# Kernel optimization log

Hardware: AMD Instinct MI355X
Metric: run time of the kernel (lower is better)

Reference implementation:

```python
import jax, jax.numpy as jnp
import numpy as np


def _logcumsumexp(x, axis):
    return jax.lax.associative_scan(jnp.logaddexp, x, axis=axis)


def _log_g(x):
    # log of g(x) = where(x>=0, x+0.5, sigmoid(x))
    return jnp.where(x >= 0, jnp.log(jax.nn.relu(x) + 0.5), -jax.nn.softplus(-x))


def _min_gru(x, Wz, bz, Wh, bh):
    # x: [B, S, D_in] -> h: [B, S, H]; log-space Heinsen parallel scan over S
    k = x @ Wz + bz                      # gate pre-activation
    log_z = -jax.nn.softplus(-k)         # log(sigmoid(k))  = log z
    log_coeffs = -jax.nn.softplus(k)     # log(1 - sigmoid(k))
    log_tilde_h = _log_g(x @ Wh + bh)    # log candidate hidden
    a_star = jnp.cumsum(log_coeffs, axis=1)
    log_h = a_star + _logcumsumexp(log_z + log_tilde_h - a_star, axis=1)
    return jnp.exp(log_h)


def setup_inputs() -> dict:
    key = jax.random.key(0)
    ks = jax.random.split(key, 7)
    B, S, D, H = 4, 4096, 1024, 1024
    s_in = 1.0 / np.sqrt(D)
    s_cat = 1.0 / np.sqrt(2 * H)
    return {
        "x": jax.random.normal(ks[0], (B, S, D), jnp.float32),
        "Wz_f": jax.random.normal(ks[1], (D, H), jnp.float32) * s_in,
        "bz_f": jnp.zeros((H,), jnp.float32),
        "Wh_f": jax.random.normal(ks[2], (D, H), jnp.float32) * s_in,
        "bh_f": jnp.zeros((H,), jnp.float32),
        "Wz_b": jax.random.normal(ks[3], (D, H), jnp.float32) * s_in,
        "bz_b": jnp.zeros((H,), jnp.float32),
        "Wh_b": jax.random.normal(ks[4], (D, H), jnp.float32) * s_in,
        "bh_b": jnp.zeros((H,), jnp.float32),
        "W_out": jax.random.normal(ks[5], (2 * H, H), jnp.float32) * s_cat,
        "b_out": jnp.zeros((H,), jnp.float32),
    }


def reference(x, Wz_f, bz_f, Wh_f, bh_f, Wz_b, bz_b, Wh_b, bh_b, W_out, b_out):
    x_rev = jnp.flip(x, axis=1)
    out_fwd = _min_gru(x, Wz_f, bz_f, Wh_f, bh_f)        # [B, S, H]
    out_bwd = _min_gru(x_rev, Wz_b, bz_b, Wh_b, bh_b)    # [B, S, H] (not re-flipped, per source)
    concat = jnp.concatenate([out_fwd, out_bwd], axis=2)  # [B, S, 2H]
    return concat @ W_out + b_out                         # [B, S, H]
```

## Files before the change

### kernel.cpp

```cpp
#include <hip/hip_runtime.h>
#include <stdint.h>

typedef __attribute__((ext_vector_type(8))) short bf16x8;
typedef __attribute__((ext_vector_type(4))) float f32x4;
typedef __attribute__((ext_vector_type(4))) unsigned short u16x4;

#define SEQ 4096

__device__ __forceinline__ float bf2f(unsigned short u) {
  union { unsigned int i; float f; } v; v.i = ((unsigned int)u) << 16; return v.f;
}
__device__ __forceinline__ unsigned short f2bf(float f) {
  union { float f; unsigned int i; } v; v.f = f;
  unsigned int u = v.i;
  u = u + 0x7FFFu + ((u >> 16) & 1u);
  return (unsigned short)(u >> 16);
}
__device__ __forceinline__ float sigm(float x) { return 1.0f / (1.0f + __expf(-x)); }


__global__ void cvt_x_kernel(const float* __restrict__ in, unsigned short* __restrict__ out, int n8) {
  int i = blockIdx.x * blockDim.x + threadIdx.x;
  int stride = gridDim.x * blockDim.x;
  for (; i < n8; i += stride) {
    const float4* p = (const float4*)in + (size_t)i * 2;
    float4 a = p[0], b = p[1];
    union { unsigned short u[8]; uint4 v; } r;
    r.u[0] = f2bf(a.x); r.u[1] = f2bf(a.y); r.u[2] = f2bf(a.z); r.u[3] = f2bf(a.w);
    r.u[4] = f2bf(b.x); r.u[5] = f2bf(b.y); r.u[6] = f2bf(b.z); r.u[7] = f2bf(b.w);
    ((uint4*)out)[i] = r.v;
  }
}

__global__ void tconvb_kernel(const float* __restrict__ s0, const float* __restrict__ s1,
                              const float* __restrict__ s2, const float* __restrict__ s3,
                              const float* __restrict__ s4, unsigned short* __restrict__ WT4,
                              unsigned short* __restrict__ WTout) {
  __shared__ float t[32][33];
  int z = blockIdx.z;
  const float* src; unsigned short* dst; int K, k0;
  if (z < 4) {
    src = (z == 0) ? s0 : (z == 1) ? s1 : (z == 2) ? s2 : s3;
    dst = WT4 + (size_t)z * 1048576; K = 1024; k0 = blockIdx.y * 32;
  } else {
    src = s4; dst = WTout; K = 2048; k0 = blockIdx.y * 32 + (z - 4) * 1024;
  }
  int n0 = blockIdx.x * 32;
  int tx = threadIdx.x & 31, ty = threadIdx.x >> 5;
#pragma unroll
  for (int i = 0; i < 32; i += 8)
    t[ty + i][tx] = src[(size_t)(k0 + ty + i) * 1024 + n0 + tx];
  __syncthreads();
#pragma unroll
  for (int i = 0; i < 32; i += 8)
    dst[(size_t)(n0 + ty + i) * K + k0 + tx] = f2bf(t[tx][ty + i]);
}

__global__ void concat_bias_kernel(const float* b0, const float* b1, const float* b2,
                                   const float* b3, float* b4) {
  int i = blockIdx.x * 256 + threadIdx.x;
  const float* p = (i < 1024) ? b0 : (i < 2048) ? b1 : (i < 3072) ? b2 : b3;
  b4[i] = p[i & 1023];
}

template <int MODE>
__device__ __forceinline__ void store_frag(const f32x4& v, const float* bias, void* Cout,
                                           int col, int rb) {
  float bcol = bias[col];
  if (MODE == 0) {
    unsigned short* ACTp = (unsigned short*)Cout;
    bool isz = ((col >> 10) & 1) == 0;
#pragma unroll
    for (int r = 0; r < 4; ++r) {
      float x = v[r] + bcol;
      float res;
      if (isz) res = sigm(-x);
      else res = (x >= 0.f) ? (x + 0.5f) : sigm(x);
      ACTp[(size_t)(rb + r) * 4096 + col] = f2bf(res);
    }
  } else {
    float* Op = (float*)Cout;
#pragma unroll
    for (int r = 0; r < 4; ++r) Op[(size_t)(rb + r) * 1024 + col] = v[r] + bcol;
  }
}

#define DSR(D, A, OFFSTR) \
  asm volatile("ds_read_b128 %0, %1 offset:" OFFSTR : "=&v"(D) : "v"(A))

#define GLL(SRC, DIDX)                                                                  \
  __builtin_amdgcn_global_load_lds((const __attribute__((address_space(1))) void*)(SRC), \
                                   (__attribute__((address_space(3))) void*)&lds[DIDX], \
                                   16, 0, 0)

template <int MODE>
__global__ __launch_bounds__(512, 2) void gemm256_kernel(
    const unsigned short* __restrict__ A, const unsigned short* __restrict__ BT,
    const float* __restrict__ bias, void* __restrict__ Cout, int K, int NT) {
  __shared__ unsigned short lds[32768];

  const int tid = threadIdx.x;
  const int lane = tid & 63;
  const int wv = tid >> 6;
  const int wm = wv >> 2;
  const int wn = wv & 3;
  const int lo = lane & 15, hi = lane >> 4;

  const int nwg = gridDim.x;
  const int bid = blockIdx.x;
  const int cpx = nwg >> 3;
  const int sw = (bid & 7) * cpx + (bid >> 3);
  const int mt = sw / NT, nt = sw - mt * NT;
  const int m0 = mt << 8, n0 = nt << 8;

  const int srow = tid >> 2;
  const int skb = (((tid & 3) ^ ((tid >> 3) & 3)) << 4);
  const unsigned short* pA0 = A + (size_t)(m0 + srow) * K + (skb >> 1);
  const unsigned short* pA1 = pA0 + (size_t)128 * K;
  const unsigned short* pB0 = BT + (size_t)(n0 + srow) * K + (skb >> 1);
  const unsigned short* pB1 = pB0 + (size_t)128 * K;
  const int dstBase = wv << 9;

#define STAGE(KT, BUF)                                     \
  do {                                                     \
    const int ko_ = (KT) << 5;                             \
    GLL(pA0 + ko_, (BUF) * 8192 + dstBase);                \
    GLL(pA1 + ko_, (BUF) * 8192 + 4096 + dstBase);         \
    GLL(pB0 + ko_, 16384 + (BUF) * 8192 + dstBase);        \
    GLL(pB1 + ko_, 16384 + (BUF) * 8192 + 4096 + dstBase); \
  } while (0)

  f32x4 acc[8][4];
#pragma unroll
  for (int i = 0; i < 8; ++i)
#pragma unroll
    for (int j = 0; j < 4; ++j) acc[i][j] = (f32x4){0.f, 0.f, 0.f, 0.f};

  const int swz = ((lo >> 1) & 3) << 4;
  const int kof = ((hi << 4) ^ swz) >> 1;
  const unsigned ldsBase = (unsigned)(unsigned long long)&lds[0];
  const unsigned aByte = ldsBase + (unsigned)((((wm * 128 + lo) * 32) + kof) << 1);
  const unsigned bByte = ldsBase + 32768u + (unsigned)((((wn * 64 + lo) * 32) + kof) << 1);

  const int nT = K >> 5;
  STAGE(0, 0);
  for (int kt = 0; kt < nT; ++kt) {
    const int buf = kt & 1;
    if (kt + 1 < nT) {
      STAGE(kt + 1, buf ^ 1);
      asm volatile("s_waitcnt vmcnt(4)" ::: "memory");
    } else {
      asm volatile("s_waitcnt vmcnt(0)" ::: "memory");
    }
    __builtin_amdgcn_s_barrier();

    const unsigned aA = aByte + (unsigned)(buf << 14);
    const unsigned bA = bByte + (unsigned)(buf << 14);
    bf16x8 af0, af1, af2, af3, af4, af5, af6, af7, bf0, bf1, bf2, bf3;
    DSR(af0, aA, "0");    DSR(af1, aA, "1024");
    DSR(af2, aA, "2048"); DSR(af3, aA, "3072");
    DSR(af4, aA, "4096"); DSR(af5, aA, "5120");
    DSR(af6, aA, "6144"); DSR(af7, aA, "7168");
    DSR(bf0, bA, "0");    DSR(bf1, bA, "1024");
    DSR(bf2, bA, "2048"); DSR(bf3, bA, "3072");
    asm volatile("s_waitcnt lgkmcnt(0)" ::: "memory");
    __builtin_amdgcn_sched_barrier(0);
    __builtin_amdgcn_s_setprio(1);
#define MM(MI, NI) \
    acc[MI][NI] = __builtin_amdgcn_mfma_f32_16x16x32_bf16(af##MI, bf##NI, acc[MI][NI], 0, 0, 0)
    MM(0, 0); MM(0, 1); MM(0, 2); MM(0, 3);
    MM(1, 0); MM(1, 1); MM(1, 2); MM(1, 3);
    MM(2, 0); MM(2, 1); MM(2, 2); MM(2, 3);
    MM(3, 0); MM(3, 1); MM(3, 2); MM(3, 3);
    MM(4, 0); MM(4, 1); MM(4, 2); MM(4, 3);
    MM(5, 0); MM(5, 1); MM(5, 2); MM(5, 3);
    MM(6, 0); MM(6, 1); MM(6, 2); MM(6, 3);
    MM(7, 0); MM(7, 1); MM(7, 2); MM(7, 3);
#undef MM
    __builtin_amdgcn_s_setprio(0);
    __builtin_amdgcn_sched_barrier(0);
    __builtin_amdgcn_s_barrier();
  }
#undef STAGE

#pragma unroll
  for (int mi = 0; mi < 8; ++mi)
#pragma unroll
    for (int ni = 0; ni < 4; ++ni)
      store_frag<MODE>(acc[mi][ni], bias, Cout,
                       n0 + wn * 64 + ni * 16 + lo,
                       m0 + wm * 128 + mi * 16 + hi * 4);
}

template <int MODE>
__global__ __launch_bounds__(512, 2) void gemm128_kernel(
    const unsigned short* __restrict__ A, const unsigned short* __restrict__ BT,
    const float* __restrict__ bias, void* __restrict__ Cout, int K, int NT) {
  __shared__ unsigned short lds[24576];

  const int tid = threadIdx.x;
  const int lane = tid & 63;
  const int wv = tid >> 6;
  const int wm = wv >> 2;
  const int wn = wv & 3;
  const int lo = lane & 15, hi = lane >> 4;

  const int nwg = gridDim.x;
  const int bid = blockIdx.x;
  const int cpx = nwg >> 3;
  const int sw = (bid & 7) * cpx + (bid >> 3);
  const int mt = sw / NT, nt = sw - mt * NT;
  const int m0 = mt << 7, n0 = nt << 8;

  const int srow = tid >> 2;
  const int skb = (((tid & 3) ^ ((tid >> 3) & 3)) << 4);
  const unsigned short* pA0 = A + (size_t)(m0 + srow) * K + (skb >> 1);
  const unsigned short* pB0 = BT + (size_t)(n0 + srow) * K + (skb >> 1);
  const unsigned short* pB1 = pB0 + (size_t)128 * K;
  const int dstBase = wv << 9;

#define STAGE(KT, BUF)                                    \
  do {                                                    \
    const int ko_ = (KT) << 5;                            \
    GLL(pA0 + ko_, (BUF) * 4096 + dstBase);               \
    GLL(pB0 + ko_, 8192 + (BUF) * 8192 + dstBase);        \
    GLL(pB1 + ko_, 8192 + (BUF) * 8192 + 4096 + dstBase); \
  } while (0)

  f32x4 acc[4][4];
#pragma unroll
  for (int i = 0; i < 4; ++i)
#pragma unroll
    for (int j = 0; j < 4; ++j) acc[i][j] = (f32x4){0.f, 0.f, 0.f, 0.f};

  const int swz = ((lo >> 1) & 3) << 4;
  const int kof = ((hi << 4) ^ swz) >> 1;
  const unsigned ldsBase = (unsigned)(unsigned long long)&lds[0];
  const unsigned aByte = ldsBase + (unsigned)((((wm * 64 + lo) * 32) + kof) << 1);
  const unsigned bByte = ldsBase + 16384u + (unsigned)((((wn * 64 + lo) * 32) + kof) << 1);

  const int nT = K >> 5;
  STAGE(0, 0);
  for (int kt = 0; kt < nT; ++kt) {
    const int buf = kt & 1;
    if (kt + 1 < nT) {
      STAGE(kt + 1, buf ^ 1);
      asm volatile("s_waitcnt vmcnt(3)" ::: "memory");
    } else {
      asm volatile("s_waitcnt vmcnt(0)" ::: "memory");
    }
    __builtin_amdgcn_s_barrier();

    const unsigned aA = aByte + (unsigned)(buf << 13);
    const unsigned bA = bByte + (unsigned)(buf << 14);
    bf16x8 af0, af1, af2, af3, bf0, bf1, bf2, bf3;
    DSR(af0, aA, "0");    DSR(af1, aA, "1024");
    DSR(af2, aA, "2048"); DSR(af3, aA, "3072");
    DSR(bf0, bA, "0");    DSR(bf1, bA, "1024");
    DSR(bf2, bA, "2048"); DSR(bf3, bA, "3072");
    asm volatile("s_waitcnt lgkmcnt(0)" ::: "memory");
    __builtin_amdgcn_sched_barrier(0);
    __builtin_amdgcn_s_setprio(1);
#define MM(MI, NI) \
    acc[MI][NI] = __builtin_amdgcn_mfma_f32_16x16x32_bf16(af##MI, bf##NI, acc[MI][NI], 0, 0, 0)
    MM(0, 0); MM(0, 1); MM(0, 2); MM(0, 3);
    MM(1, 0); MM(1, 1); MM(1, 2); MM(1, 3);
    MM(2, 0); MM(2, 1); MM(2, 2); MM(2, 3);
    MM(3, 0); MM(3, 1); MM(3, 2); MM(3, 3);
#undef MM
    __builtin_amdgcn_s_setprio(0);
    __builtin_amdgcn_sched_barrier(0);
    __builtin_amdgcn_s_barrier();
  }
#undef STAGE

#pragma unroll
  for (int mi = 0; mi < 4; ++mi)
#pragma unroll
    for (int ni = 0; ni < 4; ++ni)
      store_frag<MODE>(acc[mi][ni], bias, Cout,
                       n0 + wn * 64 + ni * 16 + lo,
                       m0 + wm * 64 + mi * 16 + hi * 4);
}


__global__ __launch_bounds__(256) void scan1v_kernel(const unsigned short* __restrict__ ACT,
                                                     float* __restrict__ CHA,
                                                     float* __restrict__ CHB) {
  int chunk = blockIdx.x & 63;
  int b = (blockIdx.x >> 6) & 3;
  int dir = blockIdx.x >> 8;
  int c4 = threadIdx.x * 4;
  size_t colA = (size_t)dir * 2048 + c4;
  float Ap[4] = {1.f, 1.f, 1.f, 1.f};
  float Bv[4] = {0.f, 0.f, 0.f, 0.f};
  int t0 = chunk * 64;
  for (int i = 0; i < 64; ++i) {
    int t = t0 + i;
    int s = dir ? (SEQ - 1 - t) : t;
    size_t base = ((size_t)b * SEQ + s) * 4096 + colA;
    u16x4 av = *(const u16x4*)&ACT[base];
    u16x4 gv = *(const u16x4*)&ACT[base + 1024];
#pragma unroll
    for (int j = 0; j < 4; ++j) {
      float a = bf2f(av[j]), g = bf2f(gv[j]);
      Bv[j] = a * Bv[j] + (1.f - a) * g;
      Ap[j] *= a;
    }
  }
  size_t o = ((size_t)(dir * 4 + b) * 64 + chunk) * 1024 + c4;
  *(float4*)&CHA[o] = (float4){Ap[0], Ap[1], Ap[2], Ap[3]};
  *(float4*)&CHB[o] = (float4){Bv[0], Bv[1], Bv[2], Bv[3]};
}

__global__ __launch_bounds__(256) void scan_phase2_kernel(const float* __restrict__ CHA,
                                                          const float* __restrict__ CHB,
                                                          float* __restrict__ HINIT) {
  int idx = blockIdx.x * 256 + threadIdx.x;
  int c = idx & 1023;
  int db = idx >> 10;
  float h = 0.f;
  for (int ck = 0; ck < 64; ++ck) {
    size_t o = ((size_t)db * 64 + ck) * 1024 + c;
    HINIT[o] = h;
    h = CHA[o] * h + CHB[o];
  }
}

__global__ __launch_bounds__(256) void scan3v_kernel(const unsigned short* __restrict__ ACT,
                                                     const float* __restrict__ HINIT,
                                                     unsigned short* __restrict__ HCAT) {
  int chunk = blockIdx.x & 63;
  int b = (blockIdx.x >> 6) & 3;
  int dir = blockIdx.x >> 8;
  int c4 = threadIdx.x * 4;
  size_t colA = (size_t)dir * 2048 + c4;
  float4 h0 = *(const float4*)&HINIT[((size_t)(dir * 4 + b) * 64 + chunk) * 1024 + c4];
  float h[4] = {h0.x, h0.y, h0.z, h0.w};
  int t0 = chunk * 64;
  for (int i = 0; i < 64; ++i) {
    int t = t0 + i;
    int s = dir ? (SEQ - 1 - t) : t;
    size_t base = ((size_t)b * SEQ + s) * 4096 + colA;
    u16x4 av = *(const u16x4*)&ACT[base];
    u16x4 gv = *(const u16x4*)&ACT[base + 1024];
    u16x4 out;
#pragma unroll
    for (int j = 0; j < 4; ++j) {
      float a = bf2f(av[j]), g = bf2f(gv[j]);
      h[j] = a * h[j] + (1.f - a) * g;
      out[j] = f2bf(h[j]);
    }
    *(u16x4*)&HCAT[((size_t)b * SEQ + t) * 2048 + dir * 1024 + c4] = out;
  }
}


extern "C" void kernel_launch(void* const* d_in, const int* in_sizes, int n_in,
                              void* d_out, int out_size, void* d_ws, size_t ws_size,
                              hipStream_t stream) {
  (void)in_sizes; (void)n_in; (void)out_size; (void)ws_size;
  const float* x     = (const float*)d_in[0];
  const float* Wz_f  = (const float*)d_in[1];
  const float* bz_f  = (const float*)d_in[2];
  const float* Wh_f  = (const float*)d_in[3];
  const float* bh_f  = (const float*)d_in[4];
  const float* Wz_b  = (const float*)d_in[5];
  const float* bz_b  = (const float*)d_in[6];
  const float* Wh_b  = (const float*)d_in[7];
  const float* bh_b  = (const float*)d_in[8];
  const float* W_out = (const float*)d_in[9];
  const float* b_out = (const float*)d_in[10];

  char* ws = (char*)d_ws;
  size_t off = 0;
  auto alloc = [&](size_t bytes) {
    char* p = ws + off;
    off = (off + bytes + 255) & ~(size_t)255;
    return p;
  };
  const size_t M = 16384;
  unsigned short* xb    = (unsigned short*)alloc(M * 1024 * 2);
  unsigned short* WT4   = (unsigned short*)alloc(4096ull * 1024 * 2);
  unsigned short* WTout = (unsigned short*)alloc(1024ull * 2048 * 2);
  unsigned short* ACT   = (unsigned short*)alloc(M * 4096 * 2);
  unsigned short* HCAT  = (unsigned short*)alloc(M * 2048 * 2);
  float* CHA   = (float*)alloc(524288ull * 4);
  float* CHB   = (float*)alloc(524288ull * 4);
  float* HINIT = (float*)alloc(524288ull * 4);
  float* b4    = (float*)alloc(4096 * 4);

  cvt_x_kernel<<<2048, 256, 0, stream>>>(x, xb, (int)(M * 1024 / 8));

  tconvb_kernel<<<dim3(32, 32, 6), 256, 0, stream>>>(Wz_f, Wh_f, Wz_b, Wh_b, W_out, WT4, WTout);
  concat_bias_kernel<<<16, 256, 0, stream>>>(bz_f, bh_f, bz_b, bh_b, b4);

  gemm256_kernel<0><<<1024, 512, 0, stream>>>(xb, WT4, b4, (void*)ACT, 1024, 16);

  scan1v_kernel<<<512, 256, 0, stream>>>(ACT, CHA, CHB);
  scan_phase2_kernel<<<32, 256, 0, stream>>>(CHA, CHB, HINIT);
  scan3v_kernel<<<512, 256, 0, stream>>>(ACT, HINIT, HCAT);

  gemm128_kernel<1><<<512, 512, 0, stream>>>(HCAT, WTout, b_out, d_out, 2048, 4);
}
```

Baseline: 336.3 us.

## Triple-buffer gemm256 LDS and split B-tile prefetch mid-MFMA loop

Converts the main projection GEMM from double to triple buffering in LDS (96 KB), prefetching two k-tiles ahead. The A-tile loads are issued before the barrier and the B-tile loads between two halves of the MFMA block, so global loads overlap compute better. This adds LDS pressure, since two blocks per CU need 192 KB, and makes the vmcnt accounting and buffer rotation more fragile.

```diff
diff --git a/kernel.cpp b/kernel.cpp
--- a/kernel.cpp
+++ b/kernel.cpp
@@ -93,11 +93,10 @@
                                    (__attribute__((address_space(3))) void*)&lds[DIDX], \
                                    16, 0, 0)
 
-template <int MODE>
-__global__ __launch_bounds__(512, 2) void gemm256_kernel(
+__global__ __launch_bounds__(512, 2) void gemm256p_kernel(
     const unsigned short* __restrict__ A, const unsigned short* __restrict__ BT,
     const float* __restrict__ bias, void* __restrict__ Cout, int K, int NT) {
-  __shared__ unsigned short lds[32768];
+  __shared__ unsigned short lds[49152];
 
   const int tid = threadIdx.x;
   const int lane = tid & 63;
@@ -121,13 +120,17 @@
   const unsigned short* pB1 = pB0 + (size_t)128 * K;
   const int dstBase = wv << 9;
 
-#define STAGE(KT, BUF)                                     \
-  do {                                                     \
-    const int ko_ = (KT) << 5;                             \
-    GLL(pA0 + ko_, (BUF) * 8192 + dstBase);                \
-    GLL(pA1 + ko_, (BUF) * 8192 + 4096 + dstBase);         \
-    GLL(pB0 + ko_, 16384 + (BUF) * 8192 + dstBase);        \
-    GLL(pB1 + ko_, 16384 + (BUF) * 8192 + 4096 + dstBase); \
+#define STAGE_A(KT, BUFO)                           \
+  do {                                              \
+    const int ko_ = (KT) << 5;                      \
+    GLL(pA0 + ko_, (BUFO) + dstBase);               \
+    GLL(pA1 + ko_, (BUFO) + 4096 + dstBase);        \
+  } while (0)
+#define STAGE_B(KT, BUFO)                           \
+  do {                                              \
+    const int ko_ = (KT) << 5;                      \
+    GLL(pB0 + ko_, (BUFO) + 8192 + dstBase);        \
+    GLL(pB1 + ko_, (BUFO) + 8192 + 4096 + dstBase); \
   } while (0)
 
   f32x4 acc[8][4];
@@ -140,22 +143,27 @@
   const int kof = ((hi << 4) ^ swz) >> 1;
   const unsigned ldsBase = (unsigned)(unsigned long long)&lds[0];
   const unsigned aByte = ldsBase + (unsigned)((((wm * 128 + lo) * 32) + kof) << 1);
-  const unsigned bByte = ldsBase + 32768u + (unsigned)((((wn * 64 + lo) * 32) + kof) << 1);
+  const unsigned bByte = ldsBase + 16384u + (unsigned)((((wn * 64 + lo) * 32) + kof) << 1);
 
   const int nT = K >> 5;
-  STAGE(0, 0);
-  for (int kt = 0; kt < nT; ++kt) {
-    const int buf = kt & 1;
-    if (kt + 1 < nT) {
-      STAGE(kt + 1, buf ^ 1);
+  STAGE_A(0, 0); STAGE_B(0, 0);
+  STAGE_A(1, 16384); STAGE_B(1, 16384);
+
+  int bufo = 0;
+  int sbufo = 32768;
+  for (int t = 0; t < nT; ++t) {
+    if (t + 2 < nT) {
+      STAGE_A(t + 2, sbufo);
+      asm volatile("s_waitcnt vmcnt(6)" ::: "memory");
+    } else if (t + 1 < nT) {
       asm volatile("s_waitcnt vmcnt(4)" ::: "memory");
     } else {
       asm volatile("s_waitcnt vmcnt(0)" ::: "memory");
     }
     __builtin_amdgcn_s_barrier();
 
-    const unsigned aA = aByte + (unsigned)(buf << 14);
-    const unsigned bA = bByte + (unsigned)(buf << 14);
+    const unsigned aA = aByte + (unsigned)(bufo << 1);
+    const unsigned bA = bByte + (unsigned)(bufo << 1);
     bf16x8 af0, af1, af2, af3, af4, af5, af6, af7, bf0, bf1, bf2, bf3;
     DSR(af0, aA, "0");    DSR(af1, aA, "1024");
     DSR(af2, aA, "2048"); DSR(af3, aA, "3072");
@@ -168,29 +176,38 @@
     __builtin_amdgcn_s_setprio(1);
 #define MM(MI, NI) \
     acc[MI][NI] = __builtin_amdgcn_mfma_f32_16x16x32_bf16(af##MI, bf##NI, acc[MI][NI], 0, 0, 0)
-    MM(0, 0); MM(0, 1); MM(0, 2); MM(0, 3);
-    MM(1, 0); MM(1, 1); MM(1, 2); MM(1, 3);
-    MM(2, 0); MM(2, 1); MM(2, 2); MM(2, 3);
-    MM(3, 0); MM(3, 1); MM(3, 2); MM(3, 3);
-    MM(4, 0); MM(4, 1); MM(4, 2); MM(4, 3);
-    MM(5, 0); MM(5, 1); MM(5, 2); MM(5, 3);
-    MM(6, 0); MM(6, 1); MM(6, 2); MM(6, 3);
-    MM(7, 0); MM(7, 1); MM(7, 2); MM(7, 3);
+    MM(0, 0); MM(0, 1); MM(1, 0); MM(1, 1);
+    MM(2, 0); MM(2, 1); MM(3, 0); MM(3, 1);
+    MM(4, 0); MM(4, 1); MM(5, 0); MM(5, 1);
+    MM(6, 0); MM(6, 1); MM(7, 0); MM(7, 1);
+    __builtin_amdgcn_s_setprio(0);
+    __builtin_amdgcn_sched_barrier(0);
+
+    if (t + 2 < nT) STAGE_B(t + 2, sbufo);
+    __builtin_amdgcn_s_setprio(1);
+    MM(0, 2); MM(0, 3); MM(1, 2); MM(1, 3);
+    MM(2, 2); MM(2, 3); MM(3, 2); MM(3, 3);
+    MM(4, 2); MM(4, 3); MM(5, 2); MM(5, 3);
+    MM(6, 2); MM(6, 3); MM(7, 2); MM(7, 3);
 #undef MM
     __builtin_amdgcn_s_setprio(0);
     __builtin_amdgcn_sched_barrier(0);
     __builtin_amdgcn_s_barrier();
-  }
-#undef STAGE
+
+    bufo += 16384;  if (bufo == 49152) bufo = 0;
+    sbufo += 16384; if (sbufo == 49152) sbufo = 0;
+  }
 
 #pragma unroll
   for (int mi = 0; mi < 8; ++mi)
 #pragma unroll
     for (int ni = 0; ni < 4; ++ni)
-      store_frag<MODE>(acc[mi][ni], bias, Cout,
-                       n0 + wn * 64 + ni * 16 + lo,
-                       m0 + wm * 128 + mi * 16 + hi * 4);
-}
+      store_frag<0>(acc[mi][ni], bias, Cout,
+                    n0 + wn * 64 + ni * 16 + lo,
+                    m0 + wm * 128 + mi * 16 + hi * 4);
+}
+#undef STAGE_A
+#undef STAGE_B
 
 template <int MODE>
 __global__ __launch_bounds__(512, 2) void gemm128_kernel(
@@ -395,7 +412,7 @@
   tconvb_kernel<<<dim3(32, 32, 6), 256, 0, stream>>>(Wz_f, Wh_f, Wz_b, Wh_b, W_out, WT4, WTout);
   concat_bias_kernel<<<16, 256, 0, stream>>>(bz_f, bh_f, bz_b, bh_b, b4);
 
-  gemm256_kernel<0><<<1024, 512, 0, stream>>>(xb, WT4, b4, (void*)ACT, 1024, 16);
+  gemm256p_kernel<<<1024, 512, 0, stream>>>(xb, WT4, b4, (void*)ACT, 1024, 16);
 
   scan1v_kernel<<<512, 256, 0, stream>>>(ACT, CHA, CHB);
   scan_phase2_kernel<<<32, 256, 0, stream>>>(CHA, CHB, HINIT);
```

Result: faster. 329.6 us (-2.0%).
